# Kernel optimization log

Measured on AMD Instinct MI355X. Metric: run time of the kernel, lower is better.

The kernel has to match this reference:

```python
import jax, jax.numpy as jnp
import numpy as np

COMM_DIM = 8
HIDDEN = 64
N = 2048


def setup_inputs() -> dict:
    key = jax.random.key(0)
    k_msg, k_w1, k_b1, k_w2, k_b2 = jax.random.split(key, 5)
    s1 = 1.0 / np.sqrt(2 * COMM_DIM)  # torch Linear default-ish scale
    s2 = 1.0 / np.sqrt(HIDDEN)
    return {
        "messages": jax.random.normal(k_msg, (N, COMM_DIM), dtype=jnp.float32),
        "W1": jax.random.normal(k_w1, (HIDDEN, 2 * COMM_DIM), dtype=jnp.float32) * s1,
        "b1": jax.random.normal(k_b1, (HIDDEN,), dtype=jnp.float32) * s1,
        "W2": jax.random.normal(k_w2, (COMM_DIM, HIDDEN), dtype=jnp.float32) * s2,
        "b2": jax.random.normal(k_b2, (COMM_DIM,), dtype=jnp.float32) * s2,
    }


def reference(messages, W1, b1, W2, b2):
    # edge_mlp(concat([m_i, m_j])) for all ordered pairs, mean over j != i.
    # Linear1 on the concat splits: concat([mi,mj]) @ W1^T = mi @ W1[:,:D]^T + mj @ W1[:,D:]^T
    n = messages.shape[0]
    X1 = jnp.einsum('nd,hd->nh', messages, W1[:, :COMM_DIM])   # [N, H] contribution of m_i
    X2 = jnp.einsum('nd,hd->nh', messages, W1[:, COMM_DIM:])   # [N, H] contribution of m_j
    # pairwise hidden: [N, N, H] (the dominant, memory-bound intermediate)
    H = jax.nn.relu(X1[:, None, :] + X2[None, :, :] + b1)
    S = H.sum(axis=1)                                          # [N, H] sum over all j (incl. j==i)
    D = jax.nn.relu(X1 + X2 + b1)                              # [N, H] the j==i diagonal term
    # agg_i = sum_{j!=i} (relu(...) @ W2^T + b2); then divide by (N-1)
    agg = jnp.einsum('nh,dh->nd', S - D, W2) + (n - 1) * b2
    return agg / (n - 1)
```

## Files before the change

kernel.cpp:

```cpp
#include <hip/hip_runtime.h>


#define NN 2048
#define HH 64
#define DD 8

#define ITILES 32
#define JCHUNKS 32
#define JCHUNK (NN / JCHUNKS)
#define INV_SCALE (0.5f / (float)(NN - 1))

__global__ void prep_kernel(const float* __restrict__ msg,
                            const float* __restrict__ W1,
                            const float* __restrict__ b1,
                            float* __restrict__ A,
                            float* __restrict__ X2,
                            float* __restrict__ out) {
    int idx = blockIdx.x * blockDim.x + threadIdx.x;
    if (idx < NN * DD) out[idx] = 0.f;
    int i = idx >> 6;
    int h = idx & 63;
    const float4* m4 = (const float4*)(msg + i * DD);
    const float4* w4 = (const float4*)(W1 + h * (2 * DD));
    float4 m0 = m4[0], m1 = m4[1];
    float4 w0 = w4[0], w1 = w4[1], w2 = w4[2], w3 = w4[3];
    float x1 = m0.x * w0.x + m0.y * w0.y + m0.z * w0.z + m0.w * w0.w
             + m1.x * w1.x + m1.y * w1.y + m1.z * w1.z + m1.w * w1.w;
    float x2 = m0.x * w2.x + m0.y * w2.y + m0.z * w2.z + m0.w * w2.w
             + m1.x * w3.x + m1.y * w3.y + m1.z * w3.z + m1.w * w3.w;
    A[idx]  = x1 + b1[h];
    X2[idx] = x2;
}

__global__ void __launch_bounds__(256, 4)
pair_fused(const float* __restrict__ A,
           const float* __restrict__ X2,
           const float* __restrict__ W2,
           const float* __restrict__ b2,
           float* __restrict__ out) {
    __shared__ float4 sX2[JCHUNK * 16];
    __shared__ float  T[64][68];
    __shared__ float4 sSXv[16];

    int it = blockIdx.x & (ITILES - 1);
    int jc = blockIdx.x >> 5;
    int hq = threadIdx.x & 15;
    int il = threadIdx.x >> 4;
    int h0 = hq * 4;
    int i0 = it * 64 + il * 4;
    bool des = (jc == it);

    {
        const float4* X2v = (const float4*)X2 + jc * JCHUNK * 16;
#pragma unroll
        for (int r = 0; r < 4; ++r) {
            int t = threadIdx.x + r * 256;
            sX2[t] = X2v[t];
        }
    }

    float a[4][4];
#pragma unroll
    for (int k = 0; k < 4; ++k) {
        float4 av = *(const float4*)&A[(i0 + k) * HH + h0];
        a[k][0] = av.x; a[k][1] = av.y; a[k][2] = av.z; a[k][3] = av.w;
    }
    float acc[4][4];
#pragma unroll
    for (int k = 0; k < 4; ++k)
#pragma unroll
        for (int hh = 0; hh < 4; ++hh)
            acc[k][hh] = 0.f;

    __syncthreads();

#pragma unroll 4
    for (int j = 0; j < JCHUNK; ++j) {
        float4 x = sX2[j * 16 + hq];
#pragma unroll
        for (int k = 0; k < 4; ++k) {
            acc[k][0] += __builtin_fabsf(a[k][0] + x.x);
            acc[k][1] += __builtin_fabsf(a[k][1] + x.y);
            acc[k][2] += __builtin_fabsf(a[k][2] + x.z);
            acc[k][3] += __builtin_fabsf(a[k][3] + x.w);
        }
    }

    const float* sX2f = (const float*)sX2;

    if (threadIdx.x < 64) {
        float s0 = 0.f, s1 = 0.f, s2 = 0.f, s3 = 0.f;
#pragma unroll 8
        for (int j = 0; j < JCHUNK; j += 4) {
            s0 += sX2f[(j + 0) * 64 + threadIdx.x];
            s1 += sX2f[(j + 1) * 64 + threadIdx.x];
            s2 += sX2f[(j + 2) * 64 + threadIdx.x];
            s3 += sX2f[(j + 3) * 64 + threadIdx.x];
        }
        ((float*)sSXv)[threadIdx.x] = (s0 + s1) + (s2 + s3);
    }

#pragma unroll
    for (int k = 0; k < 4; ++k) {
        float t0 = acc[k][0], t1 = acc[k][1], t2 = acc[k][2], t3 = acc[k][3];
        if (des) {
            int jl = il * 4 + k;
            float z0 = a[k][0] + sX2f[jl * 64 + h0 + 0];
            float z1 = a[k][1] + sX2f[jl * 64 + h0 + 1];
            float z2 = a[k][2] + sX2f[jl * 64 + h0 + 2];
            float z3 = a[k][3] + sX2f[jl * 64 + h0 + 3];
            t0 += (float)NN * a[k][0] - 2.f * (z0 > 0.f ? z0 : 0.f);
            t1 += (float)NN * a[k][1] - 2.f * (z1 > 0.f ? z1 : 0.f);
            t2 += (float)NN * a[k][2] - 2.f * (z2 > 0.f ? z2 : 0.f);
            t3 += (float)NN * a[k][3] - 2.f * (z3 > 0.f ? z3 : 0.f);
        }
        *(float4*)&T[il * 4 + k][h0] = make_float4(t0, t1, t2, t3);
    }
    __syncthreads();

    {
        int iL = threadIdx.x >> 3;
        int d  = threadIdx.x & 7;
        const float4* w2v = (const float4*)W2;
        float s0 = 0.f, s1 = 0.f, c = 0.f;
#pragma unroll
        for (int hb = 0; hb < 16; ++hb) {
            float4 w  = w2v[d * 16 + hb];
            float4 t0 = *(const float4*)&T[iL][hb * 4];
            float4 t1 = *(const float4*)&T[iL + 32][hb * 4];
            float4 sx = sSXv[hb];
            s0 += t0.x * w.x + t0.y * w.y + t0.z * w.z + t0.w * w.w;
            s1 += t1.x * w.x + t1.y * w.y + t1.z * w.z + t1.w * w.w;
            c  += sx.x * w.x + sx.y * w.y + sx.z * w.z + sx.w * w.w;
        }
        float v0 = (s0 + c) * INV_SCALE;
        float v1 = (s1 + c) * INV_SCALE;
        if (des) {
            float bv = b2[d];
            v0 += bv;
            v1 += bv;
        }
        int ibase = it * 64;
        atomicAdd(&out[(ibase + iL) * DD + d], v0);
        atomicAdd(&out[(ibase + iL + 32) * DD + d], v1);
    }
}

extern "C" void kernel_launch(void* const* d_in, const int* in_sizes, int n_in,
                              void* d_out, int out_size, void* d_ws, size_t ws_size,
                              hipStream_t stream) {
    const float* msg = (const float*)d_in[0];
    const float* W1  = (const float*)d_in[1];
    const float* b1  = (const float*)d_in[2];
    const float* W2  = (const float*)d_in[3];
    const float* b2  = (const float*)d_in[4];
    float* out = (float*)d_out;

    float* ws = (float*)d_ws;
    float* A  = ws;
    float* X2 = ws + NN * HH;

    prep_kernel<<<(NN * HH) / 256, 256, 0, stream>>>(msg, W1, b1, A, X2, out);
    pair_fused<<<ITILES * JCHUNKS, 256, 0, stream>>>(A, X2, W2, b2, out);
}
```

Baseline: 83.28 us.

## Fuse first-layer projection into pair kernel and enlarge i-tile to 128

```diff
diff --git a/kernel.cpp b/kernel.cpp
--- a/kernel.cpp
+++ b/kernel.cpp
@@ -5,88 +5,106 @@
 #define HH 64
 #define DD 8
 
-#define ITILES 32
-#define JCHUNKS 32
-#define JCHUNK (NN / JCHUNKS)
+#define ITILE 128
+#define ITILES (NN / ITILE)
+#define JCHUNK 64
+#define JCHUNKS (NN / JCHUNK)
 #define INV_SCALE (0.5f / (float)(NN - 1))
 
-__global__ void prep_kernel(const float* __restrict__ msg,
-                            const float* __restrict__ W1,
-                            const float* __restrict__ b1,
-                            float* __restrict__ A,
-                            float* __restrict__ X2,
-                            float* __restrict__ out) {
-    int idx = blockIdx.x * blockDim.x + threadIdx.x;
-    if (idx < NN * DD) out[idx] = 0.f;
-    int i = idx >> 6;
-    int h = idx & 63;
-    const float4* m4 = (const float4*)(msg + i * DD);
-    const float4* w4 = (const float4*)(W1 + h * (2 * DD));
-    float4 m0 = m4[0], m1 = m4[1];
-    float4 w0 = w4[0], w1 = w4[1], w2 = w4[2], w3 = w4[3];
-    float x1 = m0.x * w0.x + m0.y * w0.y + m0.z * w0.z + m0.w * w0.w
-             + m1.x * w1.x + m1.y * w1.y + m1.z * w1.z + m1.w * w1.w;
-    float x2 = m0.x * w2.x + m0.y * w2.y + m0.z * w2.z + m0.w * w2.w
-             + m1.x * w3.x + m1.y * w3.y + m1.z * w3.z + m1.w * w3.w;
-    A[idx]  = x1 + b1[h];
-    X2[idx] = x2;
+__device__ __forceinline__ float dot8(const float4 m0, const float4 m1,
+                                      const float4 w0, const float4 w1) {
+    return m0.x * w0.x + m0.y * w0.y + m0.z * w0.z + m0.w * w0.w
+         + m1.x * w1.x + m1.y * w1.y + m1.z * w1.z + m1.w * w1.w;
 }
 
-__global__ void __launch_bounds__(256, 4)
-pair_fused(const float* __restrict__ A,
-           const float* __restrict__ X2,
-           const float* __restrict__ W2,
-           const float* __restrict__ b2,
-           float* __restrict__ out) {
-    __shared__ float4 sX2[JCHUNK * 16];
-    __shared__ float  T[64][68];
+__global__ void zero_out(float* __restrict__ out) {
+    int idx = blockIdx.x * 256 + threadIdx.x;
+    ((float4*)out)[idx] = make_float4(0.f, 0.f, 0.f, 0.f);
+}
+
+__global__ void __launch_bounds__(256, 2)
+fused(const float* __restrict__ msg,
+      const float* __restrict__ W1,
+      const float* __restrict__ b1,
+      const float* __restrict__ W2,
+      const float* __restrict__ b2,
+      float* __restrict__ out) {
+    __shared__ float  sX2f[JCHUNK * HH];
+    __shared__ float  T[ITILE][68];
     __shared__ float4 sSXv[16];
 
     int it = blockIdx.x & (ITILES - 1);
-    int jc = blockIdx.x >> 5;
+    int jc = blockIdx.x >> 4;
     int hq = threadIdx.x & 15;
     int il = threadIdx.x >> 4;
     int h0 = hq * 4;
-    int i0 = it * 64 + il * 4;
-    bool des = (jc == it);
+    int i0 = it * ITILE + il * 8;
+    int myChunk = it * 2 + (il >> 3);
+    bool des = (myChunk == jc);
 
+    const float4* mv = (const float4*)msg;
+
+    float a[8][4];
     {
-        const float4* X2v = (const float4*)X2 + jc * JCHUNK * 16;
+        float4 mr[8][2];
 #pragma unroll
-        for (int r = 0; r < 4; ++r) {
-            int t = threadIdx.x + r * 256;
-            sX2[t] = X2v[t];
+        for (int k = 0; k < 8; ++k) {
+            mr[k][0] = mv[(i0 + k) * 2];
+            mr[k][1] = mv[(i0 + k) * 2 + 1];
+        }
+#pragma unroll
+        for (int hh = 0; hh < 4; ++hh) {
+            const float4* w4 = (const float4*)(W1 + (h0 + hh) * 16);
+            float4 wa = w4[0], wb = w4[1];
+            float bv = b1[h0 + hh];
+#pragma unroll
+            for (int k = 0; k < 8; ++k)
+                a[k][hh] = dot8(mr[k][0], mr[k][1], wa, wb) + bv;
         }
     }
 
-    float a[4][4];
+    {
+        int j0 = jc * 64 + il * 4;
+        float4 n0a = mv[(j0 + 0) * 2], n0b = mv[(j0 + 0) * 2 + 1];
+        float4 n1a = mv[(j0 + 1) * 2], n1b = mv[(j0 + 1) * 2 + 1];
+        float4 n2a = mv[(j0 + 2) * 2], n2b = mv[(j0 + 2) * 2 + 1];
+        float4 n3a = mv[(j0 + 3) * 2], n3b = mv[(j0 + 3) * 2 + 1];
+        float x2v[4][4];
 #pragma unroll
-    for (int k = 0; k < 4; ++k) {
-        float4 av = *(const float4*)&A[(i0 + k) * HH + h0];
-        a[k][0] = av.x; a[k][1] = av.y; a[k][2] = av.z; a[k][3] = av.w;
+        for (int hh = 0; hh < 4; ++hh) {
+            const float4* w4 = (const float4*)(W1 + (h0 + hh) * 16);
+            float4 wc = w4[2], wd = w4[3];
+            x2v[0][hh] = dot8(n0a, n0b, wc, wd);
+            x2v[1][hh] = dot8(n1a, n1b, wc, wd);
+            x2v[2][hh] = dot8(n2a, n2b, wc, wd);
+            x2v[3][hh] = dot8(n3a, n3b, wc, wd);
+        }
+#pragma unroll
+        for (int k = 0; k < 4; ++k)
+            *(float4*)&sX2f[(il * 4 + k) * HH + h0] =
+                make_float4(x2v[k][0], x2v[k][1], x2v[k][2], x2v[k][3]);
     }
-    float acc[4][4];
+
+    float acc[8][4];
 #pragma unroll
-    for (int k = 0; k < 4; ++k)
+    for (int k = 0; k < 8; ++k)
 #pragma unroll
         for (int hh = 0; hh < 4; ++hh)
             acc[k][hh] = 0.f;
 
     __syncthreads();
 
-#pragma unroll 4
+#pragma unroll 2
     for (int j = 0; j < JCHUNK; ++j) {
-        float4 x = sX2[j * 16 + hq];
+        float4 x = *(const float4*)&sX2f[j * HH + h0];
 #pragma unroll
-        for (int k = 0; k < 4; ++k) {
+        for (int k = 0; k < 8; ++k) {
             acc[k][0] += __builtin_fabsf(a[k][0] + x.x);
             acc[k][1] += __builtin_fabsf(a[k][1] + x.y);
             acc[k][2] += __builtin_fabsf(a[k][2] + x.z);
             acc[k][3] += __builtin_fabsf(a[k][3] + x.w);
         }
     }
-
-    const float* sX2f = (const float*)sX2;
 
     if (threadIdx.x < 64) {
         float s0 = 0.f, s1 = 0.f, s2 = 0.f, s3 = 0.f;
@@ -101,10 +119,10 @@
     }
 
 #pragma unroll
-    for (int k = 0; k < 4; ++k) {
+    for (int k = 0; k < 8; ++k) {
         float t0 = acc[k][0], t1 = acc[k][1], t2 = acc[k][2], t3 = acc[k][3];
         if (des) {
-            int jl = il * 4 + k;
+            int jl = (il & 7) * 8 + k;
             float z0 = a[k][0] + sX2f[jl * 64 + h0 + 0];
             float z1 = a[k][1] + sX2f[jl * 64 + h0 + 1];
             float z2 = a[k][2] + sX2f[jl * 64 + h0 + 2];
@@ -114,7 +132,7 @@
             t2 += (float)NN * a[k][2] - 2.f * (z2 > 0.f ? z2 : 0.f);
             t3 += (float)NN * a[k][3] - 2.f * (z3 > 0.f ? z3 : 0.f);
         }
-        *(float4*)&T[il * 4 + k][h0] = make_float4(t0, t1, t2, t3);
+        *(float4*)&T[il * 8 + k][h0] = make_float4(t0, t1, t2, t3);
     }
     __syncthreads();
 
@@ -122,27 +140,33 @@
         int iL = threadIdx.x >> 3;
         int d  = threadIdx.x & 7;
         const float4* w2v = (const float4*)W2;
-        float s0 = 0.f, s1 = 0.f, c = 0.f;
+        float s0 = 0.f, s1 = 0.f, s2 = 0.f, s3 = 0.f, c = 0.f;
 #pragma unroll
         for (int hb = 0; hb < 16; ++hb) {
             float4 w  = w2v[d * 16 + hb];
             float4 t0 = *(const float4*)&T[iL][hb * 4];
             float4 t1 = *(const float4*)&T[iL + 32][hb * 4];
+            float4 t2 = *(const float4*)&T[iL + 64][hb * 4];
+            float4 t3 = *(const float4*)&T[iL + 96][hb * 4];
             float4 sx = sSXv[hb];
             s0 += t0.x * w.x + t0.y * w.y + t0.z * w.z + t0.w * w.w;
             s1 += t1.x * w.x + t1.y * w.y + t1.z * w.z + t1.w * w.w;
+            s2 += t2.x * w.x + t2.y * w.y + t2.z * w.z + t2.w * w.w;
+            s3 += t3.x * w.x + t3.y * w.y + t3.z * w.z + t3.w * w.w;
             c  += sx.x * w.x + sx.y * w.y + sx.z * w.z + sx.w * w.w;
         }
         float v0 = (s0 + c) * INV_SCALE;
         float v1 = (s1 + c) * INV_SCALE;
-        if (des) {
-            float bv = b2[d];
-            v0 += bv;
-            v1 += bv;
-        }
-        int ibase = it * 64;
-        atomicAdd(&out[(ibase + iL) * DD + d], v0);
+        float v2 = (s2 + c) * INV_SCALE;
+        float v3 = (s3 + c) * INV_SCALE;
+        float bv = b2[d];
+        if (jc == it * 2)     { v0 += bv; v1 += bv; }
+        if (jc == it * 2 + 1) { v2 += bv; v3 += bv; }
+        int ibase = it * ITILE;
+        atomicAdd(&out[(ibase + iL) * DD + d],      v0);
         atomicAdd(&out[(ibase + iL + 32) * DD + d], v1);
+        atomicAdd(&out[(ibase + iL + 64) * DD + d], v2);
+        atomicAdd(&out[(ibase + iL + 96) * DD + d], v3);
     }
 }
 
@@ -156,10 +180,6 @@
     const float* b2  = (const float*)d_in[4];
     float* out = (float*)d_out;
 
-    float* ws = (float*)d_ws;
-    float* A  = ws;
-    float* X2 = ws + NN * HH;
-
-    prep_kernel<<<(NN * HH) / 256, 256, 0, stream>>>(msg, W1, b1, A, X2, out);
-    pair_fused<<<ITILES * JCHUNKS, 256, 0, stream>>>(A, X2, W2, b2, out);
+    zero_out<<<(NN * DD) / (256 * 4), 256, 0, stream>>>(out);
+    fused<<<ITILES * JCHUNKS, 256, 0, stream>>>(msg, W1, b1, W2, b2, out);
 }
```

New measurement: 85.32 us. 2.4% more time.
